# Performance work log

Hardware: AMD Instinct MI355X
Metric: run time of the kernel (lower is better)

The kernel has to match this reference:

```python
import jax, jax.numpy as jnp
import numpy as np

B, T, D_IN, D_OUT, H = 2, 2048, 512, 512, 8
DK = D_OUT // H


def setup_inputs() -> dict:
    key = jax.random.key(0)
    ks = jax.random.split(key, 11)
    s = 0.02
    return {
        "q": jax.random.normal(ks[0], (B, T, D_IN), jnp.float32),
        "k": jax.random.normal(ks[1], (B, T, D_IN), jnp.float32),
        "v": jax.random.normal(ks[2], (B, T, D_IN), jnp.float32),
        "Wq": jax.random.normal(ks[3], (D_OUT, D_IN), jnp.float32) * s,
        "bq": jnp.zeros((D_OUT,), jnp.float32),
        "Wk": jax.random.normal(ks[4], (D_OUT, D_IN), jnp.float32) * s,
        "bk": jnp.zeros((D_OUT,), jnp.float32),
        "Wv": jax.random.normal(ks[5], (D_OUT, D_IN), jnp.float32) * s,
        "bv": jnp.zeros((D_OUT,), jnp.float32),
        "Wo": jax.random.normal(ks[6], (D_IN, D_OUT), jnp.float32) * s,
        "bo": jnp.zeros((D_IN,), jnp.float32),
    }


def reference(q, k, v, Wq, bq, Wk, bk, Wv, bv, Wo, bo):
    def proj(x, W, b):
        # [B,T,D_in] @ [D_in,D_out] -> [B,H,T,DK]
        return (x @ W.T + b).reshape(B, T, H, DK).transpose(0, 2, 1, 3)

    qh = proj(q, Wq, bq)
    kh = proj(k, Wk, bk)
    vh = proj(v, Wv, bv)
    # NOTE: original code applies NO 1/sqrt(d_k) scaling
    scores = jnp.einsum("bhqd,bhkd->bhqk", qh, kh)  # [B,H,T,T]
    p = jax.nn.softmax(scores, axis=-1)
    # mean-threshold sparsification: keep entries strictly above row mean
    p = jnp.where(p > p.mean(axis=-1, keepdims=True), p, jnp.zeros_like(p))
    out = jnp.einsum("bhqk,bhkd->bhqd", p, vh)  # [B,H,T,DK]
    concat = out.transpose(0, 2, 1, 3).reshape(B, T, D_OUT)
    return concat @ Wo.T + bo  # [B,T,D_IN]
```

## Files before the change

kernel.cpp:

```cpp
#include <hip/hip_runtime.h>

constexpr int B_   = 2;
constexpr int T_   = 2048;
constexpr int DIN  = 512;
constexpr int DOUT = 512;
constexpr int H_   = 8;
constexpr int DK_  = 64;

typedef float    f32x16  __attribute__((ext_vector_type(16)));
typedef short    short8v __attribute__((ext_vector_type(8)));
typedef __bf16   bf16x8  __attribute__((ext_vector_type(8)));

__device__ inline f32x16 mfma3216(short8v a, short8v b, f32x16 c) {
    return __builtin_amdgcn_mfma_f32_32x32x16_bf16(
        __builtin_bit_cast(bf16x8, a), __builtin_bit_cast(bf16x8, b), c, 0, 0, 0);
}

__device__ inline unsigned short bf16c(float f) {
    return __builtin_bit_cast(unsigned short, (__bf16)f);
}
__device__ inline float bf2f(unsigned short u) {
    return (float)__builtin_bit_cast(__bf16, u);
}
__device__ inline unsigned pk2(float lo, float hi) {
    return (unsigned)bf16c(lo) | ((unsigned)bf16c(hi) << 16);
}

__global__ __launch_bounds__(256) void wconvert_kernel(
    const float* __restrict__ Wq, const float* __restrict__ Wk,
    const float* __restrict__ Wv, const float* __restrict__ Wo,
    unsigned short* __restrict__ Wh, unsigned short* __restrict__ Wl)
{
    const int b = blockIdx.x, t = threadIdx.x;
    const int wi = b >> 6;
    const float* src = wi == 0 ? Wq : (wi == 1 ? Wk : (wi == 2 ? Wv : Wo));
    unsigned short* hi = Wh + (size_t)wi * 262144;
    unsigned short* lo = Wl + (size_t)wi * 262144;
    const size_t off = (size_t)(b & 63) * 4096;
#pragma unroll
    for (int c = 0; c < 4; ++c) {
        const size_t idx = off + (size_t)c * 1024 + (size_t)t * 4;
        const float4 x = *(const float4*)&src[idx];
        ushort4 h;
        h.x = bf16c(x.x); h.y = bf16c(x.y); h.z = bf16c(x.z); h.w = bf16c(x.w);
        *(ushort4*)&hi[idx] = h;
        ushort4 l2;
        l2.x = bf16c(x.x - bf2f(h.x));
        l2.y = bf16c(x.y - bf2f(h.y));
        l2.z = bf16c(x.z - bf2f(h.z));
        l2.w = bf16c(x.w - bf2f(h.w));
        *(ushort4*)&lo[idx] = l2;
    }
}

template<int MODE>
__device__ __forceinline__ void store_c(unsigned short* __restrict__ outb,
                                        float* __restrict__ outf,
                                        int m, int n, float v)
{
    if constexpr (MODE == 0) {
        outf[(size_t)m * DOUT + n] = v;
    } else {
        const int bb = m >> 11, t = m & (T_ - 1);
        const int hh = n >> 6,  d = n & (DK_ - 1);
        const size_t bh = (size_t)bb * H_ + hh;
        if constexpr (MODE == 1) {
            outb[(bh * T_ + t) * DK_ + d] = bf16c(v);
        } else if constexpr (MODE == 3) {
            const int kt = t >> 5, l31 = t & 31;
            const int c = d >> 4, khi = (d >> 3) & 1, e = d & 7;
            outb[(bh * 64 + kt) * 2048 + (c * 2 + khi) * 256 + l31 * 8 + e] = bf16c(v);
        } else {
            const int kt = t >> 5, kgrp = (t >> 4) & 1, khi = (t >> 3) & 1, e = t & 7;
            const int dblk = d >> 5, l31 = d & 31;
            outb[(bh * 64 + kt) * 2048 + ((kgrp * 2 + dblk) * 2 + khi) * 256 + l31 * 8 + e] = bf16c(v);
        }
    }
}

template<int MODE, bool AF32, int BN>
__device__ inline void gemm_body(
    const void* __restrict__ Av, const unsigned short* __restrict__ Bhp,
    const unsigned short* __restrict__ Blp, const float* __restrict__ bias,
    unsigned short* __restrict__ outb, float* __restrict__ outf)
{
    __shared__ unsigned short As[128 * 32];
    __shared__ unsigned short Bsh[BN * 32];
    __shared__ unsigned short Bsl[BN * 32];

    const int tid = threadIdx.x;
    const int m0 = blockIdx.y * 128, n0 = blockIdx.x * BN;
    const int lane31 = tid & 31, hi8 = (tid & 63) >> 5;
    const int wv = tid >> 6, wm = wv >> 1, wn = wv & 1;

    const int r_  = tid >> 2, pos_ = tid & 3;
    const int r2_ = r_ + 64;
    const int sw_  = pos_ ^ ((r_  >> 1) & 3);
    const int sw2_ = pos_ ^ ((r2_ >> 1) & 3);

    short8v a0r, a1r, bh0r, bl0r, bh1r, bl1r;

    auto gload = [&](int kb) {
        const int k0 = kb * 32;
        if constexpr (AF32) {
            const float* Af = (const float*)Av;
            {
                const float4 f0 = *(const float4*)&Af[(size_t)(m0 + r_) * DIN + k0 + pos_ * 8];
                const float4 f1 = *(const float4*)&Af[(size_t)(m0 + r_) * DIN + k0 + pos_ * 8 + 4];
                union { unsigned w[4]; short8v v; } u;
                u.w[0] = pk2(f0.x, f0.y); u.w[1] = pk2(f0.z, f0.w);
                u.w[2] = pk2(f1.x, f1.y); u.w[3] = pk2(f1.z, f1.w);
                a0r = u.v;
            }
            {
                const float4 f0 = *(const float4*)&Af[(size_t)(m0 + r2_) * DIN + k0 + pos_ * 8];
                const float4 f1 = *(const float4*)&Af[(size_t)(m0 + r2_) * DIN + k0 + pos_ * 8 + 4];
                union { unsigned w[4]; short8v v; } u;
                u.w[0] = pk2(f0.x, f0.y); u.w[1] = pk2(f0.z, f0.w);
                u.w[2] = pk2(f1.x, f1.y); u.w[3] = pk2(f1.z, f1.w);
                a1r = u.v;
            }
        } else {
            const unsigned short* Ab = (const unsigned short*)Av;
            a0r = *(const short8v*)&Ab[(size_t)(m0 + r_)  * DIN + k0 + pos_ * 8];
            a1r = *(const short8v*)&Ab[(size_t)(m0 + r2_) * DIN + k0 + pos_ * 8];
        }
        bh0r = *(const short8v*)&Bhp[(size_t)(n0 + r_) * DIN + k0 + pos_ * 8];
        bl0r = *(const short8v*)&Blp[(size_t)(n0 + r_) * DIN + k0 + pos_ * 8];
        if constexpr (BN == 128) {
            bh1r = *(const short8v*)&Bhp[(size_t)(n0 + r2_) * DIN + k0 + pos_ * 8];
            bl1r = *(const short8v*)&Blp[(size_t)(n0 + r2_) * DIN + k0 + pos_ * 8];
        }
    };
    auto swrite = [&]() {
        *(short8v*)((char*)As + r_  * 64 + sw_  * 16) = a0r;
        *(short8v*)((char*)As + r2_ * 64 + sw2_ * 16) = a1r;
        *(short8v*)((char*)Bsh + r_ * 64 + sw_ * 16) = bh0r;
        *(short8v*)((char*)Bsl + r_ * 64 + sw_ * 16) = bl0r;
        if constexpr (BN == 128) {
            *(short8v*)((char*)Bsh + r2_ * 64 + sw2_ * 16) = bh1r;
            *(short8v*)((char*)Bsl + r2_ * 64 + sw2_ * 16) = bl1r;
        }
    };

    f32x16 acc00 = {}, acc01 = {}, acc10 = {}, acc11 = {};

    gload(0);
    for (int kb = 0; kb < 16; ++kb) {
        swrite();
        __syncthreads();
        if (kb < 15) gload(kb + 1);
#pragma unroll
        for (int ks = 0; ks < 2; ++ks) {
            const int pos = ks * 2 + hi8;
            short8v a0, a1;
            { const int r = wm * 64 + lane31;
              a0 = *(const short8v*)((char*)As + r * 64 + ((pos ^ ((r >> 1) & 3)) << 4)); }
            { const int r = wm * 64 + 32 + lane31;
              a1 = *(const short8v*)((char*)As + r * 64 + ((pos ^ ((r >> 1) & 3)) << 4)); }
            if constexpr (BN == 64) {
                short8v b0h, b0l;
                { const int r = wn * 32 + lane31;
                  b0h = *(const short8v*)((char*)Bsh + r * 64 + ((pos ^ ((r >> 1) & 3)) << 4));
                  b0l = *(const short8v*)((char*)Bsl + r * 64 + ((pos ^ ((r >> 1) & 3)) << 4)); }
                acc00 = mfma3216(a0, b0h, acc00);
                acc00 = mfma3216(a0, b0l, acc00);
                acc10 = mfma3216(a1, b0h, acc10);
                acc10 = mfma3216(a1, b0l, acc10);
            } else {
                short8v b0h, b0l, b1h, b1l;
                { const int r = wn * 64 + lane31;
                  b0h = *(const short8v*)((char*)Bsh + r * 64 + ((pos ^ ((r >> 1) & 3)) << 4));
                  b0l = *(const short8v*)((char*)Bsl + r * 64 + ((pos ^ ((r >> 1) & 3)) << 4)); }
                { const int r = wn * 64 + 32 + lane31;
                  b1h = *(const short8v*)((char*)Bsh + r * 64 + ((pos ^ ((r >> 1) & 3)) << 4));
                  b1l = *(const short8v*)((char*)Bsl + r * 64 + ((pos ^ ((r >> 1) & 3)) << 4)); }
                acc00 = mfma3216(a0, b0h, acc00);
                acc00 = mfma3216(a0, b0l, acc00);
                acc01 = mfma3216(a0, b1h, acc01);
                acc01 = mfma3216(a0, b1l, acc01);
                acc10 = mfma3216(a1, b0h, acc10);
                acc10 = mfma3216(a1, b0l, acc10);
                acc11 = mfma3216(a1, b1h, acc11);
                acc11 = mfma3216(a1, b1l, acc11);
            }
        }
        __syncthreads();
    }

    const int nb = n0 + wn * (BN / 2) + lane31;
#pragma unroll
    for (int r = 0; r < 16; ++r) {
        const int row = (r & 3) + 8 * (r >> 2) + 4 * hi8;
        store_c<MODE>(outb, outf, m0 + wm * 64 + row,      nb, acc00[r] + bias[nb]);
        store_c<MODE>(outb, outf, m0 + wm * 64 + 32 + row, nb, acc10[r] + bias[nb]);
        if constexpr (BN == 128) {
            store_c<MODE>(outb, outf, m0 + wm * 64 + row,      nb + 32, acc01[r] + bias[nb + 32]);
            store_c<MODE>(outb, outf, m0 + wm * 64 + 32 + row, nb + 32, acc11[r] + bias[nb + 32]);
        }
    }
}

__global__ __launch_bounds__(256) void qkv_gemm(
    const float* __restrict__ q, const float* __restrict__ k, const float* __restrict__ v,
    const unsigned short* __restrict__ Wh, const unsigned short* __restrict__ Wl,
    const float* __restrict__ bq, const float* __restrict__ bk, const float* __restrict__ bv,
    unsigned short* __restrict__ Qh, unsigned short* __restrict__ Kf,
    unsigned short* __restrict__ Vf)
{
    const int z = blockIdx.z;
    if (z == 0)      gemm_body<1, true, 128>(q, Wh,          Wl,          bq, Qh, nullptr);
    else if (z == 1) gemm_body<3, true, 128>(k, Wh + 262144, Wl + 262144, bk, Kf, nullptr);
    else             gemm_body<4, true, 128>(v, Wh + 524288, Wl + 524288, bv, Vf, nullptr);
}

__global__ __launch_bounds__(256) void out_gemm(
    const unsigned short* __restrict__ A,
    const unsigned short* __restrict__ Bh, const unsigned short* __restrict__ Bl,
    const float* __restrict__ bias, float* __restrict__ out)
{
    gemm_body<0, false, 64>(A, Bh, Bl, bias, nullptr, out);
}

__global__ __launch_bounds__(512) void attn_kernel(
    const unsigned short* __restrict__ Qh, const unsigned short* __restrict__ Kf,
    const unsigned short* __restrict__ Vf, unsigned short* __restrict__ concat)
{
    __shared__ float lds_l[8][32];
    __shared__ float lds_out[4][32][64];

    const int bid = blockIdx.x;
    const int xcd = bid & 7;
    const int j   = bid >> 3;
    const int bh  = 2 * xcd + (j >> 6);
    const int qt  = j & 63;

    const int tid    = threadIdx.x;
    const int w      = tid >> 6;
    const int l      = tid & 63;
    const int lane31 = l & 31;
    const int hi     = l >> 5;

    const int q0 = qt * 32;
    const unsigned short* Qb = Qh + ((size_t)bh * T_ + q0) * DK_;

    short8v qf[4];
#pragma unroll
    for (int c = 0; c < 4; ++c)
        qf[c] = *(const short8v*)(Qb + (size_t)lane31 * DK_ + c * 16 + hi * 8);

    const unsigned short* Kw = Kf + ((size_t)bh * 64 + w * 8) * 2048 + hi * 256 + lane31 * 8;
    const unsigned short* Vw = Vf + ((size_t)bh * 64 + w * 8) * 2048 + hi * 256 + lane31 * 8;

    float lsum = 0.f;
    for (int kt = 0; kt < 8; ++kt) {
        const unsigned short* Kt = Kw + kt * 2048;
        short8v kf[4];
#pragma unroll
        for (int c = 0; c < 4; ++c)
            kf[c] = *(const short8v*)(Kt + c * 512);
        f32x16 acc = {};
#pragma unroll
        for (int c = 0; c < 4; ++c)
            acc = mfma3216(kf[c], qf[c], acc);
#pragma unroll
        for (int r = 0; r < 16; ++r)
            lsum += __expf(acc[r]);
    }
    lsum += __shfl_xor(lsum, 32);
    if (l < 32) lds_l[w][l] = lsum;
    __syncthreads();
    float ltot = 0.f;
#pragma unroll
    for (int i = 0; i < 8; ++i) ltot += lds_l[i][lane31];
    const float thr = ltot * (1.0f / 2048.0f);
    const float inv = 1.0f / ltot;

    f32x16 o0 = {}, o1 = {};
    for (int kt = 0; kt < 8; ++kt) {
        const unsigned short* Kt = Kw + kt * 2048;
        short8v kf[4];
#pragma unroll
        for (int c = 0; c < 4; ++c)
            kf[c] = *(const short8v*)(Kt + c * 512);
        f32x16 acc = {};
#pragma unroll
        for (int c = 0; c < 4; ++c)
            acc = mfma3216(kf[c], qf[c], acc);

        float p[16];
#pragma unroll
        for (int r = 0; r < 16; ++r) {
            const float e = __expf(acc[r]);
            p[r] = (e > thr) ? e : 0.f;
        }

        short8v pa[2];
#pragma unroll
        for (int h = 0; h < 2; ++h) {
            const unsigned a  = pk2(p[8 * h + 0], p[8 * h + 1]);
            const unsigned b2 = pk2(p[8 * h + 2], p[8 * h + 3]);
            const unsigned c2 = pk2(p[8 * h + 4], p[8 * h + 5]);
            const unsigned d2 = pk2(p[8 * h + 6], p[8 * h + 7]);
            const unsigned sa = (unsigned)__shfl_xor((int)a,  32);
            const unsigned sb = (unsigned)__shfl_xor((int)b2, 32);
            const unsigned sc = (unsigned)__shfl_xor((int)c2, 32);
            const unsigned sd = (unsigned)__shfl_xor((int)d2, 32);
            union { unsigned w2[4]; short8v v8; } u;
            u.w2[0] = hi ? sc : a;
            u.w2[1] = hi ? sd : b2;
            u.w2[2] = hi ? c2 : sa;
            u.w2[3] = hi ? d2 : sb;
            pa[h] = u.v8;
        }

        const unsigned short* Vt_ = Vw + kt * 2048;
#pragma unroll
        for (int h = 0; h < 2; ++h) {
            short8v vf0 = *(const short8v*)(Vt_ + (2 * h)     * 512);
            short8v vf1 = *(const short8v*)(Vt_ + (2 * h + 1) * 512);
            o0 = mfma3216(pa[h], vf0, o0);
            o1 = mfma3216(pa[h], vf1, o1);
        }
    }

    if (w >= 4) {
#pragma unroll
        for (int r = 0; r < 16; ++r) {
            const int row = (r & 3) + 8 * (r >> 2) + 4 * hi;
            lds_out[w - 4][row][lane31]      = o0[r];
            lds_out[w - 4][row][32 + lane31] = o1[r];
        }
    }
    __syncthreads();
    if (w < 4) {
#pragma unroll
        for (int r = 0; r < 16; ++r) {
            const int row = (r & 3) + 8 * (r >> 2) + 4 * hi;
            o0[r] += lds_out[w][row][lane31];
            o1[r] += lds_out[w][row][32 + lane31];
        }
    }
    __syncthreads();
    if (w >= 1 && w < 4) {
#pragma unroll
        for (int r = 0; r < 16; ++r) {
            const int row = (r & 3) + 8 * (r >> 2) + 4 * hi;
            lds_out[w - 1][row][lane31]      = o0[r];
            lds_out[w - 1][row][32 + lane31] = o1[r];
        }
    }
    __syncthreads();
    if (w == 0) {
        const int b = bh >> 3, h = bh & 7;
        unsigned short* Cb = concat + ((size_t)b * T_ + q0) * DOUT + h * DK_;
#pragma unroll
        for (int r = 0; r < 16; ++r) {
            const int row = (r & 3) + 8 * (r >> 2) + 4 * hi;
            const float iv = __shfl(inv, row);
            const float v0 = o0[r] + lds_out[0][row][lane31]
                           + lds_out[1][row][lane31] + lds_out[2][row][lane31];
            const float v1 = o1[r] + lds_out[0][row][32 + lane31]
                           + lds_out[1][row][32 + lane31] + lds_out[2][row][32 + lane31];
            Cb[(size_t)row * DOUT + lane31]      = bf16c(v0 * iv);
            Cb[(size_t)row * DOUT + 32 + lane31] = bf16c(v1 * iv);
        }
    }
}

extern "C" void kernel_launch(void* const* d_in, const int* in_sizes, int n_in,
                              void* d_out, int out_size, void* d_ws, size_t ws_size,
                              hipStream_t stream)
{
    const float* q  = (const float*)d_in[0];
    const float* k  = (const float*)d_in[1];
    const float* v  = (const float*)d_in[2];
    const float* Wq = (const float*)d_in[3];
    const float* bq = (const float*)d_in[4];
    const float* Wk = (const float*)d_in[5];
    const float* bk = (const float*)d_in[6];
    const float* Wv = (const float*)d_in[7];
    const float* bv = (const float*)d_in[8];
    const float* Wo = (const float*)d_in[9];
    const float* bo = (const float*)d_in[10];
    float* out = (float*)d_out;

    constexpr size_t M2 = 2097152;
    unsigned short* ws     = (unsigned short*)d_ws;
    unsigned short* Qh     = ws;
    unsigned short* Kf     = ws + 1 * M2;
    unsigned short* Vf     = ws + 2 * M2;
    unsigned short* concat = ws + 3 * M2;
    unsigned short* Wh     = ws + 4 * M2;
    unsigned short* Wl     = ws + 4 * M2 + 1048576;

    wconvert_kernel<<<256, 256, 0, stream>>>(Wq, Wk, Wv, Wo, Wh, Wl);
    qkv_gemm<<<dim3(4, 32, 3), 256, 0, stream>>>(q, k, v, Wh, Wl, bq, bk, bv, Qh, Kf, Vf);
    attn_kernel<<<dim3(1024), 512, 0, stream>>>(Qh, Kf, Vf, concat);
    out_gemm<<<dim3(8, 32), 256, 0, stream>>>(concat, Wh + 786432, Wl + 786432, bo, out);
}
```

Baseline: 90.40 us.

## Fold log2e into Wq, use exp2, permlane32 swap, and MFMA priority hints

Scales the Q projection weights and bias by log2(e) so the attention kernel can call the native exp2 instead of expf. It also swaps the four shfl_xor exchanges plus selects for v_permlane32_swap instructions. It splits the row-sum into four independent accumulators and wraps the MFMA groups in s_setprio hints. The aim is to cut VALU and cross-lane overhead in the exp/threshold path. Folding the scale into bf16 hi/lo weights slightly changes rounding of the Q projection.

```diff
diff --git a/kernel.cpp b/kernel.cpp
--- a/kernel.cpp
+++ b/kernel.cpp
@@ -7,6 +7,8 @@
 constexpr int H_   = 8;
 constexpr int DK_  = 64;
 
+constexpr float LOG2E = 1.44269504088896340736f;
+
 typedef float    f32x16  __attribute__((ext_vector_type(16)));
 typedef short    short8v __attribute__((ext_vector_type(8)));
 typedef __bf16   bf16x8  __attribute__((ext_vector_type(8)));
@@ -24,6 +26,9 @@
 }
 __device__ inline unsigned pk2(float lo, float hi) {
     return (unsigned)bf16c(lo) | ((unsigned)bf16c(hi) << 16);
+}
+__device__ __forceinline__ void pl32swap(unsigned &x, unsigned &y) {
+    asm("v_permlane32_swap_b32 %0, %1" : "+v"(x), "+v"(y));
 }
 
 __global__ __launch_bounds__(256) void wconvert_kernel(
@@ -36,11 +41,13 @@
     const float* src = wi == 0 ? Wq : (wi == 1 ? Wk : (wi == 2 ? Wv : Wo));
     unsigned short* hi = Wh + (size_t)wi * 262144;
     unsigned short* lo = Wl + (size_t)wi * 262144;
+    const float scl = (wi == 0) ? LOG2E : 1.0f;
     const size_t off = (size_t)(b & 63) * 4096;
 #pragma unroll
     for (int c = 0; c < 4; ++c) {
         const size_t idx = off + (size_t)c * 1024 + (size_t)t * 4;
-        const float4 x = *(const float4*)&src[idx];
+        float4 x = *(const float4*)&src[idx];
+        x.x *= scl; x.y *= scl; x.z *= scl; x.w *= scl;
         ushort4 h;
         h.x = bf16c(x.x); h.y = bf16c(x.y); h.z = bf16c(x.z); h.w = bf16c(x.w);
         *(ushort4*)&hi[idx] = h;
@@ -82,6 +89,7 @@
 __device__ inline void gemm_body(
     const void* __restrict__ Av, const unsigned short* __restrict__ Bhp,
     const unsigned short* __restrict__ Blp, const float* __restrict__ bias,
+    float bscale,
     unsigned short* __restrict__ outb, float* __restrict__ outf)
 {
     __shared__ unsigned short As[128 * 32];
@@ -192,11 +200,11 @@
 #pragma unroll
     for (int r = 0; r < 16; ++r) {
         const int row = (r & 3) + 8 * (r >> 2) + 4 * hi8;
-        store_c<MODE>(outb, outf, m0 + wm * 64 + row,      nb, acc00[r] + bias[nb]);
-        store_c<MODE>(outb, outf, m0 + wm * 64 + 32 + row, nb, acc10[r] + bias[nb]);
+        store_c<MODE>(outb, outf, m0 + wm * 64 + row,      nb, acc00[r] + bias[nb] * bscale);
+        store_c<MODE>(outb, outf, m0 + wm * 64 + 32 + row, nb, acc10[r] + bias[nb] * bscale);
         if constexpr (BN == 128) {
-            store_c<MODE>(outb, outf, m0 + wm * 64 + row,      nb + 32, acc01[r] + bias[nb + 32]);
-            store_c<MODE>(outb, outf, m0 + wm * 64 + 32 + row, nb + 32, acc11[r] + bias[nb + 32]);
+            store_c<MODE>(outb, outf, m0 + wm * 64 + row,      nb + 32, acc01[r] + bias[nb + 32] * bscale);
+            store_c<MODE>(outb, outf, m0 + wm * 64 + 32 + row, nb + 32, acc11[r] + bias[nb + 32] * bscale);
         }
     }
 }
@@ -209,9 +217,9 @@
     unsigned short* __restrict__ Vf)
 {
     const int z = blockIdx.z;
-    if (z == 0)      gemm_body<1, true, 128>(q, Wh,          Wl,          bq, Qh, nullptr);
-    else if (z == 1) gemm_body<3, true, 128>(k, Wh + 262144, Wl + 262144, bk, Kf, nullptr);
-    else             gemm_body<4, true, 128>(v, Wh + 524288, Wl + 524288, bv, Vf, nullptr);
+    if (z == 0)      gemm_body<1, true, 128>(q, Wh,          Wl,          bq, LOG2E, Qh, nullptr);
+    else if (z == 1) gemm_body<3, true, 128>(k, Wh + 262144, Wl + 262144, bk, 1.0f,  Kf, nullptr);
+    else             gemm_body<4, true, 128>(v, Wh + 524288, Wl + 524288, bv, 1.0f,  Vf, nullptr);
 }
 
 __global__ __launch_bounds__(256) void out_gemm(
@@ -219,7 +227,7 @@
     const unsigned short* __restrict__ Bh, const unsigned short* __restrict__ Bl,
     const float* __restrict__ bias, float* __restrict__ out)
 {
-    gemm_body<0, false, 64>(A, Bh, Bl, bias, nullptr, out);
+    gemm_body<0, false, 64>(A, Bh, Bl, bias, 1.0f, nullptr, out);
 }
 
 __global__ __launch_bounds__(512) void attn_kernel(
@@ -252,7 +260,7 @@
     const unsigned short* Kw = Kf + ((size_t)bh * 64 + w * 8) * 2048 + hi * 256 + lane31 * 8;
     const unsigned short* Vw = Vf + ((size_t)bh * 64 + w * 8) * 2048 + hi * 256 + lane31 * 8;
 
-    float lsum = 0.f;
+    float ls0 = 0.f, ls1 = 0.f, ls2 = 0.f, ls3 = 0.f;
     for (int kt = 0; kt < 8; ++kt) {
         const unsigned short* Kt = Kw + kt * 2048;
         short8v kf[4];
@@ -260,13 +268,20 @@
         for (int c = 0; c < 4; ++c)
             kf[c] = *(const short8v*)(Kt + c * 512);
         f32x16 acc = {};
+        __builtin_amdgcn_s_setprio(1);
 #pragma unroll
         for (int c = 0; c < 4; ++c)
             acc = mfma3216(kf[c], qf[c], acc);
-#pragma unroll
-        for (int r = 0; r < 16; ++r)
-            lsum += __expf(acc[r]);
-    }
+        __builtin_amdgcn_s_setprio(0);
+#pragma unroll
+        for (int r = 0; r < 16; r += 4) {
+            ls0 += __builtin_amdgcn_exp2f(acc[r + 0]);
+            ls1 += __builtin_amdgcn_exp2f(acc[r + 1]);
+            ls2 += __builtin_amdgcn_exp2f(acc[r + 2]);
+            ls3 += __builtin_amdgcn_exp2f(acc[r + 3]);
+        }
+    }
+    float lsum = (ls0 + ls1) + (ls2 + ls3);
     lsum += __shfl_xor(lsum, 32);
     if (l < 32) lds_l[w][l] = lsum;
     __syncthreads();
@@ -284,44 +299,44 @@
         for (int c = 0; c < 4; ++c)
             kf[c] = *(const short8v*)(Kt + c * 512);
         f32x16 acc = {};
+        __builtin_amdgcn_s_setprio(1);
 #pragma unroll
         for (int c = 0; c < 4; ++c)
             acc = mfma3216(kf[c], qf[c], acc);
+        __builtin_amdgcn_s_setprio(0);
 
         float p[16];
 #pragma unroll
         for (int r = 0; r < 16; ++r) {
-            const float e = __expf(acc[r]);
+            const float e = __builtin_amdgcn_exp2f(acc[r]);
             p[r] = (e > thr) ? e : 0.f;
         }
 
         short8v pa[2];
 #pragma unroll
         for (int h = 0; h < 2; ++h) {
-            const unsigned a  = pk2(p[8 * h + 0], p[8 * h + 1]);
-            const unsigned b2 = pk2(p[8 * h + 2], p[8 * h + 3]);
-            const unsigned c2 = pk2(p[8 * h + 4], p[8 * h + 5]);
-            const unsigned d2 = pk2(p[8 * h + 6], p[8 * h + 7]);
-            const unsigned sa = (unsigned)__shfl_xor((int)a,  32);
-            const unsigned sb = (unsigned)__shfl_xor((int)b2, 32);
-            const unsigned sc = (unsigned)__shfl_xor((int)c2, 32);
-            const unsigned sd = (unsigned)__shfl_xor((int)d2, 32);
+            unsigned a  = pk2(p[8 * h + 0], p[8 * h + 1]);
+            unsigned b2 = pk2(p[8 * h + 2], p[8 * h + 3]);
+            unsigned c2 = pk2(p[8 * h + 4], p[8 * h + 5]);
+            unsigned d2 = pk2(p[8 * h + 6], p[8 * h + 7]);
+            pl32swap(a, c2);
+            pl32swap(b2, d2);
             union { unsigned w2[4]; short8v v8; } u;
-            u.w2[0] = hi ? sc : a;
-            u.w2[1] = hi ? sd : b2;
-            u.w2[2] = hi ? c2 : sa;
-            u.w2[3] = hi ? d2 : sb;
+            u.w2[0] = a; u.w2[1] = b2; u.w2[2] = c2; u.w2[3] = d2;
             pa[h] = u.v8;
         }
 
         const unsigned short* Vt_ = Vw + kt * 2048;
-#pragma unroll
-        for (int h = 0; h < 2; ++h) {
-            short8v vf0 = *(const short8v*)(Vt_ + (2 * h)     * 512);
-            short8v vf1 = *(const short8v*)(Vt_ + (2 * h + 1) * 512);
-            o0 = mfma3216(pa[h], vf0, o0);
-            o1 = mfma3216(pa[h], vf1, o1);
-        }
+        short8v vf0 = *(const short8v*)(Vt_);
+        short8v vf1 = *(const short8v*)(Vt_ + 512);
+        short8v vf2 = *(const short8v*)(Vt_ + 1024);
+        short8v vf3 = *(const short8v*)(Vt_ + 1536);
+        __builtin_amdgcn_s_setprio(1);
+        o0 = mfma3216(pa[0], vf0, o0);
+        o1 = mfma3216(pa[0], vf1, o1);
+        o0 = mfma3216(pa[1], vf2, o0);
+        o1 = mfma3216(pa[1], vf3, o1);
+        __builtin_amdgcn_s_setprio(0);
     }
 
     if (w >= 4) {
```

After: 88.81 us. Within noise of the previous version (-1.8%).
